# Kernel tuning notes

Measured on AMD Instinct MI355X. Metric: run time of the kernel, lower is better.

## Reference

```python
import jax, jax.numpy as jnp
import numpy as np
import math

B, S, D, H = 2, 2048, 1024, 16


def setup_inputs() -> dict:
    key = jax.random.key(0)
    ks = jax.random.split(key, 5)
    sc = 0.02  # small init scale for weights
    return {
        "x": jax.random.normal(ks[0], (B, S, D), dtype=jnp.float32),
        "Wqkv_w": jax.random.normal(ks[1], (3 * D, D), dtype=jnp.float32) * sc,
        "Wqkv_b": jnp.zeros((3 * D,), jnp.float32),
        "sel_w": jax.random.normal(ks[2], (1, D), dtype=jnp.float32) * sc,
        "sel_b": jnp.zeros((1,), jnp.float32),
        "out_w": jax.random.normal(ks[3], (D, D), dtype=jnp.float32) * sc,
        "out_b": jnp.zeros((D,), jnp.float32),
    }


def reference(x, Wqkv_w, Wqkv_b, sel_w, sel_b, out_w, out_b):
    b, s, d = x.shape
    h = H
    hd = d // h
    # Wqkv projection -> (b, s, 3, h, hd)
    qkv = (x @ Wqkv_w.T + Wqkv_b).reshape(b, s, 3, h, hd)
    q, k, v = qkv[:, :, 0], qkv[:, :, 1], qkv[:, :, 2]
    scale = 1.0 / math.sqrt(hd)
    scores = jnp.einsum('bthd,bshd->bhts', q, k * scale)  # (b,h,s,s)
    causal_mask = jnp.triu(jnp.full((s, s), -10000.0, dtype=scores.dtype), 1)
    attn = jax.nn.softmax(scores + causal_mask, axis=-1)
    ctx = jnp.einsum('bhts,bshd->bthd', attn, v).reshape(b, s, d)
    attn_out = ctx @ out_w.T + out_b  # (b,s,d)
    # selection: softmax over sequence dim, scaled by sqrt(d)/8
    sel = jax.nn.softmax(x @ sel_w.T + sel_b, axis=1) * (math.sqrt(d) / 8.0)  # (b,s,1)
    # eval path: topk over sequence, gather, scatter_add into x
    kk = math.ceil(math.sqrt(s))  # 46 for s=2048
    _, idx = jax.lax.top_k(sel[..., 0], kk)  # (b,kk) indices into seq dim
    val = attn_out * sel  # (b,s,d)
    bidx = jnp.arange(b)[:, None]
    src = val[bidx, idx]  # gather -> (b,kk,d)
    y = x.at[bidx, idx].add(src)  # scatter_add
    return y
```

## Files before the change

### kernel.cpp

```cpp
#include <hip/hip_runtime.h>
#include <stdint.h>

#define BATCH 2
#define SEQ   2048
#define DIM   1024
#define NH    16
#define HD    64
#define KK    46
#define NSEL  (BATCH*KK)
#define MPAD  128
#define CHUNK 128
#define NCH   (SEQ/CHUNK)
#define QP    48
#define SPLITK 8

typedef __attribute__((ext_vector_type(8))) short short8;
typedef __attribute__((ext_vector_type(4))) float f32x4;

__device__ inline unsigned short f2bf(float f) {
  union { float f; uint32_t u; } v; v.f = f;
  uint32_t u = v.u;
  uint32_t r = u + 0x7fff + ((u >> 16) & 1);
  return (unsigned short)(r >> 16);
}
__device__ inline float bf2f(unsigned short h) {
  union { uint32_t u; float f; } v; v.u = ((uint32_t)h) << 16;
  return v.f;
}
__device__ inline uint32_t f2ord(float f) {
  union { float f; uint32_t u; } v; v.f = f;
  return (v.u & 0x80000000u) ? ~v.u : (v.u | 0x80000000u);
}

__device__ inline void gload16(const void* g, void* l) {
  __builtin_amdgcn_global_load_lds(
      (const __attribute__((address_space(1))) void*)g,
      (__attribute__((address_space(3))) void*)l, 16, 0, 0);
}

__global__ void cvtw_kernel(const float* __restrict__ wqkv, const float* __restrict__ outw,
                            unsigned short* __restrict__ wqkvb, unsigned short* __restrict__ outwb) {
  int i = (blockIdx.x * 256 + threadIdx.x) * 8;
  const int NW = 3 * DIM * DIM;
  const float* src; unsigned short* dst; int j;
  if (i < NW) { src = wqkv; dst = wqkvb; j = i; }
  else        { src = outw; dst = outwb; j = i - NW; }
  float4 a = *(const float4*)(src + j);
  float4 b = *(const float4*)(src + j + 4);
  ushort4 o0, o1;
  o0.x = f2bf(a.x); o0.y = f2bf(a.y); o0.z = f2bf(a.z); o0.w = f2bf(a.w);
  o1.x = f2bf(b.x); o1.y = f2bf(b.y); o1.z = f2bf(b.z); o1.w = f2bf(b.w);
  *(ushort4*)(dst + j)     = o0;
  *(ushort4*)(dst + j + 4) = o1;
}

__global__ __launch_bounds__(256) void cvtx_selz_kernel(const float* __restrict__ x,
                                                        unsigned short* __restrict__ xb,
                                                        const float* __restrict__ sel_w,
                                                        const float* __restrict__ sel_b,
                                                        float* __restrict__ z)
{
  int wave = threadIdx.x >> 6, lane = threadIdx.x & 63;
  int row = blockIdx.x * 4 + wave;
  const float* xr = x + (size_t)row * DIM;
  unsigned short* xo = xb + (size_t)row * DIM;
  float s = 0.f;
#pragma unroll
  for (int it = 0; it < 4; ++it) {
    int c = it * 256 + lane * 4;
    float4 xv = *(const float4*)(xr + c);
    float4 wv = *(const float4*)(sel_w + c);
    s += xv.x*wv.x + xv.y*wv.y + xv.z*wv.z + xv.w*wv.w;
    ushort4 o;
    o.x = f2bf(xv.x); o.y = f2bf(xv.y); o.z = f2bf(xv.z); o.w = f2bf(xv.w);
    *(ushort4*)(xo + c) = o;
  }
#pragma unroll
  for (int o = 32; o > 0; o >>= 1) s += __shfl_xor(s, o);
  if (lane == 0) z[row] = s + sel_b[0];
}

__global__ __launch_bounds__(256) void gemm_bt_kernel(
    const unsigned short* __restrict__ A,
    const unsigned short* __restrict__ Bw,
    const float* __restrict__ bias,
    unsigned short* __restrict__ Cout, int M, int N, int K)
{
  __shared__ unsigned short As[2][128*32];
  __shared__ unsigned short Bs[2][128*32];
  int tid  = threadIdx.x;
  int lane = tid & 63, wave = tid >> 6;
  int wr = (wave >> 1) * 64, wc = (wave & 1) * 64;

  int nwg  = gridDim.x * gridDim.y;
  int flat = blockIdx.y * gridDim.x + blockIdx.x;
  int xcd = flat & 7, i8 = flat >> 3;
  int q = nwg >> 3, r = nwg & 7;
  int tile = (xcd < r) ? (xcd * (q + 1) + i8) : (r * (q + 1) + (xcd - r) * q + i8);
  int bx = tile % gridDim.x, by = tile / gridDim.x;
  int bm = by * 128, bn = bx * 128;

  int lr = lane & 15, lk = (lane >> 4) * 8;
  int srow = lane >> 2;
  int scol = (lane & 3) * 8;

  const unsigned short* ap[2];
  const unsigned short* bp[2];
#pragma unroll
  for (int c = 0; c < 2; ++c) {
    int row = (wave * 2 + c) * 16 + srow;
    ap[c] = A  + (size_t)(bm + row) * K + scol;
    bp[c] = Bw + (size_t)(bn + row) * K + scol;
  }

  f32x4 acc[4][4] = {};
  int nt = K / 32;
#pragma unroll
  for (int c = 0; c < 2; ++c) {
    int ch = wave * 2 + c;
    gload16(ap[c], (char*)As[0] + ch * 1024 + lane * 16);
    gload16(bp[c], (char*)Bs[0] + ch * 1024 + lane * 16);
  }
  __syncthreads();

  int cur = 0;
  for (int t = 0; t < nt; ++t) {
    if (t + 1 < nt) {
      int k0 = (t + 1) * 32;
#pragma unroll
      for (int c = 0; c < 2; ++c) {
        int ch = wave * 2 + c;
        gload16(ap[c] + k0, (char*)As[cur ^ 1] + ch * 1024 + lane * 16);
        gload16(bp[c] + k0, (char*)Bs[cur ^ 1] + ch * 1024 + lane * 16);
      }
    }
    short8 af[4], bf[4];
#pragma unroll
    for (int m = 0; m < 4; ++m) af[m] = *(const short8*)&As[cur][(wr + m*16 + lr)*32 + lk];
#pragma unroll
    for (int n = 0; n < 4; ++n) bf[n] = *(const short8*)&Bs[cur][(wc + n*16 + lr)*32 + lk];
#pragma unroll
    for (int m = 0; m < 4; ++m)
#pragma unroll
      for (int n = 0; n < 4; ++n)
        acc[m][n] = __builtin_amdgcn_mfma_f32_16x16x32_bf16(af[m], bf[n], acc[m][n], 0, 0, 0);
    __syncthreads();
    cur ^= 1;
  }

  int rb = 4 * (lane >> 4);
#pragma unroll
  for (int m = 0; m < 4; ++m) {
#pragma unroll
    for (int n = 0; n < 4; ++n) {
      int col = bn + wc + n*16 + lr;
      float bv = bias[col];
#pragma unroll
      for (int i = 0; i < 4; ++i) {
        int row = bm + wr + m*16 + rb + i;
        Cout[(size_t)row * N + col] = f2bf(acc[m][n][i] + bv);
      }
    }
  }
}

template<int GATHER>
__global__ __launch_bounds__(256) void gemm_splitk_kernel(
    const unsigned short* __restrict__ A,
    const unsigned short* __restrict__ Bw,
    float* __restrict__ part, int N, int K,
    const int* __restrict__ idxp)
{
  __shared__ unsigned short As[2][128*32];
  __shared__ unsigned short Bs[2][128*32];
  int tid  = threadIdx.x;
  int lane = tid & 63, wave = tid >> 6;
  int wr = (wave >> 1) * 64, wc = (wave & 1) * 64;
  int bn = blockIdx.x * 128;
  int sk = blockIdx.z;
  int ksl = K / SPLITK;
  int kb  = sk * ksl;

  int lr = lane & 15, lk = (lane >> 4) * 8;
  int srow = lane >> 2;
  int scol = (lane & 3) * 8;

  const unsigned short* ap[2];
  const unsigned short* bp[2];
#pragma unroll
  for (int c = 0; c < 2; ++c) {
    int row = (wave * 2 + c) * 16 + srow;
    size_t arow;
    if (GATHER) {
      int bb = 0, rr = 0;
      if (row < NSEL) { bb = row / KK; rr = idxp[row]; }
      arow = (size_t)(bb * SEQ + rr);
    } else {
      arow = (size_t)row;
    }
    ap[c] = A  + arow * K + kb + scol;
    bp[c] = Bw + (size_t)(bn + row) * K + kb + scol;
  }

  f32x4 acc[4][4] = {};
  int nt = ksl / 32;
#pragma unroll
  for (int c = 0; c < 2; ++c) {
    int ch = wave * 2 + c;
    gload16(ap[c], (char*)As[0] + ch * 1024 + lane * 16);
    gload16(bp[c], (char*)Bs[0] + ch * 1024 + lane * 16);
  }
  __syncthreads();

  int cur = 0;
  for (int t = 0; t < nt; ++t) {
    if (t + 1 < nt) {
      int k0 = (t + 1) * 32;
#pragma unroll
      for (int c = 0; c < 2; ++c) {
        int ch = wave * 2 + c;
        gload16(ap[c] + k0, (char*)As[cur ^ 1] + ch * 1024 + lane * 16);
        gload16(bp[c] + k0, (char*)Bs[cur ^ 1] + ch * 1024 + lane * 16);
      }
    }
    short8 af[4], bf[4];
#pragma unroll
    for (int m = 0; m < 4; ++m) af[m] = *(const short8*)&As[cur][(wr + m*16 + lr)*32 + lk];
#pragma unroll
    for (int n = 0; n < 4; ++n) bf[n] = *(const short8*)&Bs[cur][(wc + n*16 + lr)*32 + lk];
#pragma unroll
    for (int m = 0; m < 4; ++m)
#pragma unroll
      for (int n = 0; n < 4; ++n)
        acc[m][n] = __builtin_amdgcn_mfma_f32_16x16x32_bf16(af[m], bf[n], acc[m][n], 0, 0, 0);
    __syncthreads();
    cur ^= 1;
  }

  int rb = 4 * (lane >> 4);
  float* po = part + (size_t)sk * MPAD * N;
#pragma unroll
  for (int m = 0; m < 4; ++m) {
#pragma unroll
    for (int n = 0; n < 4; ++n) {
      int col = bn + wc + n*16 + lr;
#pragma unroll
      for (int i = 0; i < 4; ++i) {
        int row = wr + m*16 + rb + i;
        po[(size_t)row * N + col] = acc[m][n][i];
      }
    }
  }
}

__global__ void qcombine_kernel(const float* __restrict__ part,
                                const float* __restrict__ bias,
                                unsigned short* __restrict__ qgb)
{
  int i = (blockIdx.x * 256 + threadIdx.x) * 4;
  int col = i & (DIM - 1);
  float4 a = *(const float4*)(bias + col);
#pragma unroll
  for (int sk = 0; sk < SPLITK; ++sk) {
    float4 p = *(const float4*)(part + (size_t)sk * MPAD * DIM + i);
    a.x += p.x; a.y += p.y; a.z += p.z; a.w += p.w;
  }
  ushort4 o;
  o.x = f2bf(a.x); o.y = f2bf(a.y); o.z = f2bf(a.z); o.w = f2bf(a.w);
  *(ushort4*)(qgb + i) = o;
}

__global__ __launch_bounds__(256) void topk_kernel(const float* __restrict__ z,
                                                   float* __restrict__ sel,
                                                   int* __restrict__ idxout,
                                                   int* __restrict__ rowmap)
{
  int b = blockIdx.x, t = threadIdx.x;
  int lane = t & 63, wid = t >> 6;
  __shared__ int   hist[256];
  __shared__ float fred[4];
  __shared__ int   ired[4];
  __shared__ int   s_B, s_need;
  __shared__ float s_mx, s_sum;

  int s0 = t * 8;
  float zz[8];
  uint32_t uu[8];
  {
    float4 a = *(const float4*)(z + b*SEQ + s0);
    float4 c = *(const float4*)(z + b*SEQ + s0 + 4);
    zz[0]=a.x; zz[1]=a.y; zz[2]=a.z; zz[3]=a.w;
    zz[4]=c.x; zz[5]=c.y; zz[6]=c.z; zz[7]=c.w;
  }
#pragma unroll
  for (int i = 0; i < 8; ++i) uu[i] = f2ord(zz[i]);

  float lm = zz[0];
#pragma unroll
  for (int i = 1; i < 8; ++i) lm = fmaxf(lm, zz[i]);
#pragma unroll
  for (int o = 32; o > 0; o >>= 1) lm = fmaxf(lm, __shfl_xor(lm, o));
  if (lane == 0) fred[wid] = lm;
  __syncthreads();
  if (t == 0) s_mx = fmaxf(fmaxf(fred[0], fred[1]), fmaxf(fred[2], fred[3]));
  __syncthreads();
  float mx = s_mx;

  float pp[8];
  float ls = 0.f;
#pragma unroll
  for (int i = 0; i < 8; ++i) { pp[i] = __expf(zz[i] - mx); ls += pp[i]; }
#pragma unroll
  for (int o = 32; o > 0; o >>= 1) ls += __shfl_xor(ls, o);
  if (lane == 0) fred[wid] = ls;
  __syncthreads();
  if (t == 0) s_sum = fred[0] + fred[1] + fred[2] + fred[3];
  __syncthreads();
  float sscale = 4.0f / s_sum;
#pragma unroll
  for (int i = 0; i < 8; ++i) sel[b*SEQ + s0 + i] = pp[i] * sscale;

  uint32_t pref = 0;
  int need = KK;
#pragma unroll
  for (int pass = 0; pass < 4; ++pass) {
    int shift = 24 - pass * 8;
    uint32_t maskhi = pass ? (0xFFFFFFFFu << (shift + 8)) : 0u;
    hist[t] = 0;
    __syncthreads();
#pragma unroll
    for (int i = 0; i < 8; ++i) {
      if ((uu[i] & maskhi) == pref)
        atomicAdd(&hist[(uu[i] >> shift) & 255], 1);
    }
    __syncthreads();
    if (t < 64) {
      int c0 = hist[t*4], c1 = hist[t*4+1], c2 = hist[t*4+2], c3 = hist[t*4+3];
      int sl = c0 + c1 + c2 + c3;
      int suf = sl;
#pragma unroll
      for (int off = 1; off < 64; off <<= 1) {
        int o = __shfl_down(suf, off);
        if (lane + off < 64) suf += o;
      }
      int above = suf - sl;
      if (above < need && above + sl >= need) {
        int cum = above;
        int cs[4] = {c0, c1, c2, c3};
#pragma unroll
        for (int k = 3; k >= 0; --k) {
          if (cum < need && cum + cs[k] >= need) {
            s_B = t*4 + k;
            s_need = need - cum;
            break;
          }
          cum += cs[k];
        }
      }
    }
    __syncthreads();
    pref |= ((uint32_t)s_B) << shift;
    need = s_need;
    __syncthreads();
  }
  uint32_t T = pref;

  int cgt = 0, ceq = 0;
#pragma unroll
  for (int i = 0; i < 8; ++i) { cgt += (uu[i] > T); ceq += (uu[i] == T); }
  int pack = (cgt << 12) | ceq;
  int inc = pack;
#pragma unroll
  for (int off = 1; off < 64; off <<= 1) {
    int o = __shfl_up(inc, off);
    if (lane >= off) inc += o;
  }
  if (lane == 63) ired[wid] = inc;
  __syncthreads();
  int wbase = 0;
  if (wid == 1) wbase = ired[0];
  else if (wid == 2) wbase = ired[0] + ired[1];
  else if (wid == 3) wbase = ired[0] + ired[1] + ired[2];
  int ex = wbase + inc - pack;
  int g = ex >> 12, e = ex & 0xFFF;
#pragma unroll
  for (int i = 0; i < 8; ++i) {
    int s = s0 + i;
    bool isgt = uu[i] > T;
    bool iseq = uu[i] == T;
    int rank = -1;
    if (isgt) rank = g + (e < need ? e : need);
    else if (iseq && e < need) rank = g + e;
    if (rank >= 0) {
      int j = b*KK + rank;
      idxout[j] = s;
      rowmap[b*SEQ + s] = j;
    } else {
      rowmap[b*SEQ + s] = -1;
    }
    g += isgt; e += iseq;
  }
}

__global__ __launch_bounds__(256) void attn_chunk_kernel(
    const unsigned short* __restrict__ qgb,
    const unsigned short* __restrict__ kvb,
    const int* __restrict__ idx,
    float* __restrict__ Opart,
    float* __restrict__ mpart,
    float* __restrict__ lpart)
{
  int h = blockIdx.x, b = blockIdx.y, kc = blockIdx.z;
  int t = threadIdx.x, lane = t & 63, w = t >> 6;
  int lr = lane & 15, hk = lane >> 4;

  __shared__ unsigned short Qs[QP][72];
  __shared__ union { unsigned short Ks[CHUNK][72]; unsigned short ps[QP][136]; } U;
  __shared__ unsigned short Vt[HD][134];
  __shared__ int   rsi[QP];
  __shared__ float wred[4][QP];
  __shared__ float wsum[4][QP];

  if (t < QP) rsi[t] = (t < KK) ? idx[b*KK + t] : -1;
  for (int i = t; i < QP*8; i += 256) {
    int q = i >> 3, c8 = (i & 7) * 8;
    uint4 v;
    if (q < KK) v = *(const uint4*)(qgb + (size_t)(b*KK + q)*DIM + h*HD + c8);
    else        { v.x = 0; v.y = 0; v.z = 0; v.w = 0; }
    *(uint4*)&Qs[q][c8] = v;
  }
  for (int i = t; i < CHUNK*8; i += 256) {
    int r = i >> 3, c8 = (i & 7) * 8;
    *(uint4*)&U.Ks[r][c8] =
      *(const uint4*)(kvb + ((size_t)(b*SEQ + kc*CHUNK + r))*2048 + h*HD + c8);
  }
  for (int i = t; i < CHUNK*8; i += 256) {
    int r = i >> 3, d8 = (i & 7) * 8;
    uint4 v = *(const uint4*)(kvb + ((size_t)(b*SEQ + kc*CHUNK + r))*2048 + DIM + h*HD + d8);
    const unsigned short* pv = (const unsigned short*)&v;
#pragma unroll
    for (int j = 0; j < 8; ++j) Vt[d8 + j][r] = pv[j];
  }
  __syncthreads();

  short8 af[3][2], bfr[2][2];
#pragma unroll
  for (int m = 0; m < 3; ++m)
#pragma unroll
    for (int kk = 0; kk < 2; ++kk)
      af[m][kk] = *(const short8*)&Qs[m*16 + lr][kk*32 + hk*8];
#pragma unroll
  for (int j = 0; j < 2; ++j)
#pragma unroll
    for (int kk = 0; kk < 2; ++kk)
      bfr[j][kk] = *(const short8*)&U.Ks[(2*w + j)*16 + lr][kk*32 + hk*8];
  f32x4 acc[3][2] = {};
#pragma unroll
  for (int kk = 0; kk < 2; ++kk)
#pragma unroll
    for (int m = 0; m < 3; ++m)
#pragma unroll
      for (int j = 0; j < 2; ++j)
        acc[m][j] = __builtin_amdgcn_mfma_f32_16x16x32_bf16(af[m][kk], bfr[j][kk], acc[m][j], 0, 0, 0);

  float s[3][2][4];
  float rmax[3][4];
#pragma unroll
  for (int m = 0; m < 3; ++m)
#pragma unroll
    for (int reg = 0; reg < 4; ++reg) {
      int row = m*16 + hk*4 + reg;
      int rq = rsi[row];
      float mx = -3e38f;
#pragma unroll
      for (int j = 0; j < 2; ++j) {
        int gkey = kc*CHUNK + (2*w + j)*16 + lr;
        float v = acc[m][j][reg] * 0.125f;
        if (gkey > rq) v = -3e38f;
        s[m][j][reg] = v;
        mx = fmaxf(mx, v);
      }
#pragma unroll
      for (int o = 1; o < 16; o <<= 1) mx = fmaxf(mx, __shfl_xor(mx, o));
      rmax[m][reg] = mx;
    }
  if (lr == 0) {
#pragma unroll
    for (int m = 0; m < 3; ++m)
#pragma unroll
      for (int reg = 0; reg < 4; ++reg)
        wred[w][m*16 + hk*4 + reg] = rmax[m][reg];
  }
  __syncthreads();

  float rsum[3][4];
#pragma unroll
  for (int m = 0; m < 3; ++m)
#pragma unroll
    for (int reg = 0; reg < 4; ++reg) {
      int row = m*16 + hk*4 + reg;
      float gm = fmaxf(fmaxf(wred[0][row], wred[1][row]), fmaxf(wred[2][row], wred[3][row]));
      gm = fmaxf(gm, -1e37f);
      float sum = 0.f;
#pragma unroll
      for (int j = 0; j < 2; ++j) {
        float p = __expf(s[m][j][reg] - gm);
        sum += p;
        U.ps[row][(2*w + j)*16 + lr] = f2bf(p);
      }
#pragma unroll
      for (int o = 1; o < 16; o <<= 1) sum += __shfl_xor(sum, o);
      rsum[m][reg] = sum;
      rmax[m][reg] = gm;
    }
  if (lr == 0) {
#pragma unroll
    for (int m = 0; m < 3; ++m)
#pragma unroll
      for (int reg = 0; reg < 4; ++reg)
        wsum[w][m*16 + hk*4 + reg] = rsum[m][reg];
  }
  __syncthreads();

  if (w == 0 && lr == 0) {
    size_t base = ((size_t)(b*NH + h)*NCH + kc)*KK;
#pragma unroll
    for (int m = 0; m < 3; ++m)
#pragma unroll
      for (int reg = 0; reg < 4; ++reg) {
        int row = m*16 + hk*4 + reg;
        if (row < KK) {
          float L = wsum[0][row] + wsum[1][row] + wsum[2][row] + wsum[3][row];
          mpart[base + row] = rmax[m][reg];
          lpart[base + row] = L;
        }
      }
  }

  f32x4 acc2[3] = {};
#pragma unroll
  for (int kt = 0; kt < 4; ++kt) {
    short8 bv = *(const short8*)&Vt[w*16 + lr][kt*32 + hk*8];
#pragma unroll
    for (int m = 0; m < 3; ++m) {
      short8 av = *(const short8*)&U.ps[m*16 + lr][kt*32 + hk*8];
      acc2[m] = __builtin_amdgcn_mfma_f32_16x16x32_bf16(av, bv, acc2[m], 0, 0, 0);
    }
  }
  size_t obase = (((size_t)(b*NH + h)*NCH + kc)*KK)*HD;
#pragma unroll
  for (int m = 0; m < 3; ++m)
#pragma unroll
    for (int reg = 0; reg < 4; ++reg) {
      int q = m*16 + hk*4 + reg;
      if (q < KK) Opart[obase + (size_t)q*HD + w*16 + lr] = acc2[m][reg];
    }
}

__global__ __launch_bounds__(64) void attn_combine_kernel(
    const float* __restrict__ Opart,
    const float* __restrict__ mpart,
    const float* __restrict__ lpart,
    unsigned short* __restrict__ ctxg)
{
  int h = blockIdx.x, j = blockIdx.y;
  int b = j / KK, q = j % KK;
  int d = threadIdx.x;
  size_t mb = (size_t)(b*NH + h)*NCH;
  float M = -3e38f;
#pragma unroll
  for (int c = 0; c < NCH; ++c) M = fmaxf(M, mpart[(mb + c)*KK + q]);
  float L = 0.f, o = 0.f;
#pragma unroll
  for (int c = 0; c < NCH; ++c) {
    float f = __expf(mpart[(mb + c)*KK + q] - M);
    L += lpart[(mb + c)*KK + q] * f;
    o = fmaf(Opart[((mb + c)*KK + q)*HD + d], f, o);
  }
  ctxg[(size_t)j*DIM + h*HD + d] = f2bf(o / L);
}

__global__ void fused_out_kernel(const float* __restrict__ x,
                                 const float* __restrict__ apart,
                                 const float* __restrict__ out_b,
                                 const float* __restrict__ sel,
                                 const int* __restrict__ rowmap,
                                 float* __restrict__ out)
{
  size_t i = ((size_t)blockIdx.x * 256 + threadIdx.x) * 4;
  int row = (int)(i >> 10);
  int col = (int)(i & 1023);
  float4 v = *(const float4*)(x + i);
  int j = rowmap[row];
  if (j >= 0) {
    float s = sel[row];
    float4 a = *(const float4*)(out_b + col);
#pragma unroll
    for (int sk = 0; sk < SPLITK; ++sk) {
      float4 p = *(const float4*)(apart + ((size_t)sk * MPAD + j) * DIM + col);
      a.x += p.x; a.y += p.y; a.z += p.z; a.w += p.w;
    }
    v.x += a.x * s; v.y += a.y * s; v.z += a.z * s; v.w += a.w * s;
  }
  *(float4*)(out + i) = v;
}

extern "C" void kernel_launch(void* const* d_in, const int* in_sizes, int n_in,
                              void* d_out, int out_size, void* d_ws, size_t ws_size,
                              hipStream_t stream)
{
  (void)in_sizes; (void)n_in; (void)out_size; (void)ws_size;
  const float* x      = (const float*)d_in[0];
  const float* Wqkv_w = (const float*)d_in[1];
  const float* Wqkv_b = (const float*)d_in[2];
  const float* sel_w  = (const float*)d_in[3];
  const float* sel_b  = (const float*)d_in[4];
  const float* out_w  = (const float*)d_in[5];
  const float* out_b  = (const float*)d_in[6];
  float* out = (float*)d_out;
  char* ws = (char*)d_ws;

  unsigned short* xb    = (unsigned short*)(ws);
  unsigned short* wqkvb = (unsigned short*)(ws + (8u  << 20));
  unsigned short* outwb = (unsigned short*)(ws + (14u << 20));
  unsigned short* kvb   = (unsigned short*)(ws + (16u << 20));
  float* z      = (float*)(ws + (32u << 20));
  float* sel    = (float*)(ws + (32u << 20) + (16u << 10));
  int*   idx    = (int*)  (ws + (32u << 20) + (32u << 10));
  int*   rowmap = (int*)  (ws + (32u << 20) + (36u << 10));
  unsigned short* ctxg = (unsigned short*)(ws + (33u << 20) + (256u << 10));
  unsigned short* qgb  = (unsigned short*)(ws + (33u << 20) + (512u << 10));
  float* Opart = (float*)(ws + (35u << 20));
  float* mpart = (float*)(ws + (42u << 20));
  float* lpart = (float*)(ws + (42u << 20) + (256u << 10));
  float* qpart = (float*)(ws + (44u << 20));
  float* apart = (float*)(ws + (48u << 20));

  cvtw_kernel<<<2048, 256, 0, stream>>>(Wqkv_w, out_w, wqkvb, outwb);
  cvtx_selz_kernel<<<BATCH*SEQ/4, 256, 0, stream>>>(x, xb, sel_w, sel_b, z);
  topk_kernel<<<BATCH, 256, 0, stream>>>(z, sel, idx, rowmap);

  dim3 gkv(2048/128, (BATCH*SEQ)/128);
  gemm_bt_kernel<<<gkv, 256, 0, stream>>>(xb, wqkvb + (size_t)DIM*DIM, Wqkv_b + DIM,
                                          kvb, BATCH*SEQ, 2*DIM, DIM);

  dim3 gsk(DIM/128, 1, SPLITK);
  gemm_splitk_kernel<1><<<gsk, 256, 0, stream>>>(xb, wqkvb, qpart, DIM, DIM, idx);
  qcombine_kernel<<<MPAD*DIM/1024, 256, 0, stream>>>(qpart, Wqkv_b, qgb);

  dim3 gac(NH, BATCH, NCH);
  attn_chunk_kernel<<<gac, 256, 0, stream>>>(qgb, kvb, idx, Opart, mpart, lpart);
  dim3 gcb(NH, NSEL);
  attn_combine_kernel<<<gcb, 64, 0, stream>>>(Opart, mpart, lpart, ctxg);

  gemm_splitk_kernel<0><<<gsk, 256, 0, stream>>>(ctxg, outwb, apart, DIM, DIM, nullptr);

  fused_out_kernel<<<BATCH*SEQ*DIM/1024, 256, 0, stream>>>(x, apart, out_b, sel, rowmap, out);
}
```

Baseline: 85.70 us.

## Merge prep kernels, fuse KV and Q GEMMs, copy x early and fix only selected rows

Merges the weight conversion and the x conversion/selection-logit kernels into one launch, and that launch also writes x straight into the output. The KV projection GEMM and the gathered split-K Q GEMM now run in a single launch, removing separate launches and letting the small Q work overlap the large GEMM. The final full-tensor pass that re-read x and a rowmap is replaced by a small kernel that updates only the 92 selected rows, so the rowmap writes are gone. The cost is that the prep kernel now writes the whole output as well, and the fused GEMM grid puts two kinds of blocks with very different lengths in one launch.

```diff
diff --git a/kernel.cpp b/kernel.cpp
--- a/kernel.cpp
+++ b/kernel.cpp
@@ -38,138 +38,324 @@
       (__attribute__((address_space(3))) void*)l, 16, 0, 0);
 }
 
-__global__ void cvtw_kernel(const float* __restrict__ wqkv, const float* __restrict__ outw,
-                            unsigned short* __restrict__ wqkvb, unsigned short* __restrict__ outwb) {
-  int i = (blockIdx.x * 256 + threadIdx.x) * 8;
-  const int NW = 3 * DIM * DIM;
-  const float* src; unsigned short* dst; int j;
-  if (i < NW) { src = wqkv; dst = wqkvb; j = i; }
-  else        { src = outw; dst = outwb; j = i - NW; }
-  float4 a = *(const float4*)(src + j);
-  float4 b = *(const float4*)(src + j + 4);
-  ushort4 o0, o1;
-  o0.x = f2bf(a.x); o0.y = f2bf(a.y); o0.z = f2bf(a.z); o0.w = f2bf(a.w);
-  o1.x = f2bf(b.x); o1.y = f2bf(b.y); o1.z = f2bf(b.z); o1.w = f2bf(b.w);
-  *(ushort4*)(dst + j)     = o0;
-  *(ushort4*)(dst + j + 4) = o1;
-}
-
-__global__ __launch_bounds__(256) void cvtx_selz_kernel(const float* __restrict__ x,
-                                                        unsigned short* __restrict__ xb,
-                                                        const float* __restrict__ sel_w,
-                                                        const float* __restrict__ sel_b,
-                                                        float* __restrict__ z)
-{
-  int wave = threadIdx.x >> 6, lane = threadIdx.x & 63;
-  int row = blockIdx.x * 4 + wave;
-  const float* xr = x + (size_t)row * DIM;
-  unsigned short* xo = xb + (size_t)row * DIM;
-  float s = 0.f;
-#pragma unroll
-  for (int it = 0; it < 4; ++it) {
-    int c = it * 256 + lane * 4;
-    float4 xv = *(const float4*)(xr + c);
-    float4 wv = *(const float4*)(sel_w + c);
-    s += xv.x*wv.x + xv.y*wv.y + xv.z*wv.z + xv.w*wv.w;
-    ushort4 o;
-    o.x = f2bf(xv.x); o.y = f2bf(xv.y); o.z = f2bf(xv.z); o.w = f2bf(xv.w);
-    *(ushort4*)(xo + c) = o;
-  }
-#pragma unroll
-  for (int o = 32; o > 0; o >>= 1) s += __shfl_xor(s, o);
-  if (lane == 0) z[row] = s + sel_b[0];
-}
-
-__global__ __launch_bounds__(256) void gemm_bt_kernel(
-    const unsigned short* __restrict__ A,
-    const unsigned short* __restrict__ Bw,
-    const float* __restrict__ bias,
-    unsigned short* __restrict__ Cout, int M, int N, int K)
+__global__ __launch_bounds__(256) void prep_kernel(
+    const float* __restrict__ wqkv, const float* __restrict__ outw,
+    unsigned short* __restrict__ wqkvb, unsigned short* __restrict__ outwb,
+    const float* __restrict__ x, unsigned short* __restrict__ xb,
+    const float* __restrict__ sel_w, const float* __restrict__ sel_b,
+    float* __restrict__ z, float* __restrict__ out)
+{
+  if (blockIdx.x < 2048) {
+    int i = (blockIdx.x * 256 + threadIdx.x) * 8;
+    const int NW = 3 * DIM * DIM;
+    const float* src; unsigned short* dst; int j;
+    if (i < NW) { src = wqkv; dst = wqkvb; j = i; }
+    else        { src = outw; dst = outwb; j = i - NW; }
+    float4 a = *(const float4*)(src + j);
+    float4 b = *(const float4*)(src + j + 4);
+    ushort4 o0, o1;
+    o0.x = f2bf(a.x); o0.y = f2bf(a.y); o0.z = f2bf(a.z); o0.w = f2bf(a.w);
+    o1.x = f2bf(b.x); o1.y = f2bf(b.y); o1.z = f2bf(b.z); o1.w = f2bf(b.w);
+    *(ushort4*)(dst + j)     = o0;
+    *(ushort4*)(dst + j + 4) = o1;
+  } else {
+    int wave = threadIdx.x >> 6, lane = threadIdx.x & 63;
+    int row = (blockIdx.x - 2048) * 4 + wave;
+    const float* xr = x + (size_t)row * DIM;
+    unsigned short* xo = xb + (size_t)row * DIM;
+    float* oo = out + (size_t)row * DIM;
+    float s = 0.f;
+#pragma unroll
+    for (int it = 0; it < 4; ++it) {
+      int c = it * 256 + lane * 4;
+      float4 xv = *(const float4*)(xr + c);
+      float4 wv = *(const float4*)(sel_w + c);
+      s += xv.x*wv.x + xv.y*wv.y + xv.z*wv.z + xv.w*wv.w;
+      ushort4 o;
+      o.x = f2bf(xv.x); o.y = f2bf(xv.y); o.z = f2bf(xv.z); o.w = f2bf(xv.w);
+      *(ushort4*)(xo + c) = o;
+      *(float4*)(oo + c) = xv;
+    }
+#pragma unroll
+    for (int o = 32; o > 0; o >>= 1) s += __shfl_xor(s, o);
+    if (lane == 0) z[row] = s + sel_b[0];
+  }
+}
+
+__global__ __launch_bounds__(256) void topk_kernel(const float* __restrict__ z,
+                                                   float* __restrict__ sel,
+                                                   int* __restrict__ idxout)
+{
+  int b = blockIdx.x, t = threadIdx.x;
+  int lane = t & 63, wid = t >> 6;
+  __shared__ int   hist[256];
+  __shared__ float fred[4];
+  __shared__ int   ired[4];
+  __shared__ int   s_B, s_need;
+  __shared__ float s_mx, s_sum;
+
+  int s0 = t * 8;
+  float zz[8];
+  uint32_t uu[8];
+  {
+    float4 a = *(const float4*)(z + b*SEQ + s0);
+    float4 c = *(const float4*)(z + b*SEQ + s0 + 4);
+    zz[0]=a.x; zz[1]=a.y; zz[2]=a.z; zz[3]=a.w;
+    zz[4]=c.x; zz[5]=c.y; zz[6]=c.z; zz[7]=c.w;
+  }
+#pragma unroll
+  for (int i = 0; i < 8; ++i) uu[i] = f2ord(zz[i]);
+
+  float lm = zz[0];
+#pragma unroll
+  for (int i = 1; i < 8; ++i) lm = fmaxf(lm, zz[i]);
+#pragma unroll
+  for (int o = 32; o > 0; o >>= 1) lm = fmaxf(lm, __shfl_xor(lm, o));
+  if (lane == 0) fred[wid] = lm;
+  __syncthreads();
+  if (t == 0) s_mx = fmaxf(fmaxf(fred[0], fred[1]), fmaxf(fred[2], fred[3]));
+  __syncthreads();
+  float mx = s_mx;
+
+  float pp[8];
+  float ls = 0.f;
+#pragma unroll
+  for (int i = 0; i < 8; ++i) { pp[i] = __expf(zz[i] - mx); ls += pp[i]; }
+#pragma unroll
+  for (int o = 32; o > 0; o >>= 1) ls += __shfl_xor(ls, o);
+  if (lane == 0) fred[wid] = ls;
+  __syncthreads();
+  if (t == 0) s_sum = fred[0] + fred[1] + fred[2] + fred[3];
+  __syncthreads();
+  float sscale = 4.0f / s_sum;
+#pragma unroll
+  for (int i = 0; i < 8; ++i) sel[b*SEQ + s0 + i] = pp[i] * sscale;
+
+  uint32_t pref = 0;
+  int need = KK;
+#pragma unroll
+  for (int pass = 0; pass < 4; ++pass) {
+    int shift = 24 - pass * 8;
+    uint32_t maskhi = pass ? (0xFFFFFFFFu << (shift + 8)) : 0u;
+    hist[t] = 0;
+    __syncthreads();
+#pragma unroll
+    for (int i = 0; i < 8; ++i) {
+      if ((uu[i] & maskhi) == pref)
+        atomicAdd(&hist[(uu[i] >> shift) & 255], 1);
+    }
+    __syncthreads();
+    if (t < 64) {
+      int c0 = hist[t*4], c1 = hist[t*4+1], c2 = hist[t*4+2], c3 = hist[t*4+3];
+      int sl = c0 + c1 + c2 + c3;
+      int suf = sl;
+#pragma unroll
+      for (int off = 1; off < 64; off <<= 1) {
+        int o = __shfl_down(suf, off);
+        if (lane + off < 64) suf += o;
+      }
+      int above = suf - sl;
+      if (above < need && above + sl >= need) {
+        int cum = above;
+        int cs[4] = {c0, c1, c2, c3};
+#pragma unroll
+        for (int k = 3; k >= 0; --k) {
+          if (cum < need && cum + cs[k] >= need) {
+            s_B = t*4 + k;
+            s_need = need - cum;
+            break;
+          }
+          cum += cs[k];
+        }
+      }
+    }
+    __syncthreads();
+    pref |= ((uint32_t)s_B) << shift;
+    need = s_need;
+    __syncthreads();
+  }
+  uint32_t T = pref;
+
+  int cgt = 0, ceq = 0;
+#pragma unroll
+  for (int i = 0; i < 8; ++i) { cgt += (uu[i] > T); ceq += (uu[i] == T); }
+  int pack = (cgt << 12) | ceq;
+  int inc = pack;
+#pragma unroll
+  for (int off = 1; off < 64; off <<= 1) {
+    int o = __shfl_up(inc, off);
+    if (lane >= off) inc += o;
+  }
+  if (lane == 63) ired[wid] = inc;
+  __syncthreads();
+  int wbase = 0;
+  if (wid == 1) wbase = ired[0];
+  else if (wid == 2) wbase = ired[0] + ired[1];
+  else if (wid == 3) wbase = ired[0] + ired[1] + ired[2];
+  int ex = wbase + inc - pack;
+  int g = ex >> 12, e = ex & 0xFFF;
+#pragma unroll
+  for (int i = 0; i < 8; ++i) {
+    int s = s0 + i;
+    bool isgt = uu[i] > T;
+    bool iseq = uu[i] == T;
+    int rank = -1;
+    if (isgt) rank = g + (e < need ? e : need);
+    else if (iseq && e < need) rank = g + e;
+    if (rank >= 0) idxout[b*KK + rank] = s;
+    g += isgt; e += iseq;
+  }
+}
+
+__global__ __launch_bounds__(256) void gemms_kernel(
+    const unsigned short* __restrict__ xb,
+    const unsigned short* __restrict__ wqkvb,
+    const float* __restrict__ Wqkv_b,
+    unsigned short* __restrict__ kvb,
+    float* __restrict__ qpart,
+    const int* __restrict__ idxp)
 {
   __shared__ unsigned short As[2][128*32];
   __shared__ unsigned short Bs[2][128*32];
   int tid  = threadIdx.x;
   int lane = tid & 63, wave = tid >> 6;
   int wr = (wave >> 1) * 64, wc = (wave & 1) * 64;
-
-  int nwg  = gridDim.x * gridDim.y;
-  int flat = blockIdx.y * gridDim.x + blockIdx.x;
-  int xcd = flat & 7, i8 = flat >> 3;
-  int q = nwg >> 3, r = nwg & 7;
-  int tile = (xcd < r) ? (xcd * (q + 1) + i8) : (r * (q + 1) + (xcd - r) * q + i8);
-  int bx = tile % gridDim.x, by = tile / gridDim.x;
-  int bm = by * 128, bn = bx * 128;
-
   int lr = lane & 15, lk = (lane >> 4) * 8;
   int srow = lane >> 2;
   int scol = (lane & 3) * 8;
-
-  const unsigned short* ap[2];
-  const unsigned short* bp[2];
-#pragma unroll
-  for (int c = 0; c < 2; ++c) {
-    int row = (wave * 2 + c) * 16 + srow;
-    ap[c] = A  + (size_t)(bm + row) * K + scol;
-    bp[c] = Bw + (size_t)(bn + row) * K + scol;
-  }
-
-  f32x4 acc[4][4] = {};
-  int nt = K / 32;
-#pragma unroll
-  for (int c = 0; c < 2; ++c) {
-    int ch = wave * 2 + c;
-    gload16(ap[c], (char*)As[0] + ch * 1024 + lane * 16);
-    gload16(bp[c], (char*)Bs[0] + ch * 1024 + lane * 16);
-  }
-  __syncthreads();
-
-  int cur = 0;
-  for (int t = 0; t < nt; ++t) {
-    if (t + 1 < nt) {
-      int k0 = (t + 1) * 32;
-#pragma unroll
-      for (int c = 0; c < 2; ++c) {
-        int ch = wave * 2 + c;
-        gload16(ap[c] + k0, (char*)As[cur ^ 1] + ch * 1024 + lane * 16);
-        gload16(bp[c] + k0, (char*)Bs[cur ^ 1] + ch * 1024 + lane * 16);
-      }
-    }
-    short8 af[4], bf[4];
-#pragma unroll
-    for (int m = 0; m < 4; ++m) af[m] = *(const short8*)&As[cur][(wr + m*16 + lr)*32 + lk];
-#pragma unroll
-    for (int n = 0; n < 4; ++n) bf[n] = *(const short8*)&Bs[cur][(wc + n*16 + lr)*32 + lk];
-#pragma unroll
-    for (int m = 0; m < 4; ++m)
-#pragma unroll
-      for (int n = 0; n < 4; ++n)
-        acc[m][n] = __builtin_amdgcn_mfma_f32_16x16x32_bf16(af[m], bf[n], acc[m][n], 0, 0, 0);
+  int rb = 4 * (lane >> 4);
+
+  if (blockIdx.x < 512) {
+    const unsigned short* Bw = wqkvb + (size_t)DIM * DIM;
+    int flat = blockIdx.x;
+    int xcd = flat & 7, i8 = flat >> 3;
+    int tile = xcd * 64 + i8;
+    int bx = tile & 15, by = tile >> 4;
+    int bm = by * 128, bn = bx * 128;
+    const int K = DIM, N = 2 * DIM;
+
+    const unsigned short* ap[2];
+    const unsigned short* bp[2];
+#pragma unroll
+    for (int c = 0; c < 2; ++c) {
+      int row = (wave * 2 + c) * 16 + srow;
+      ap[c] = xb + (size_t)(bm + row) * K + scol;
+      bp[c] = Bw + (size_t)(bn + row) * K + scol;
+    }
+    f32x4 acc[4][4] = {};
+#pragma unroll
+    for (int c = 0; c < 2; ++c) {
+      int ch = wave * 2 + c;
+      gload16(ap[c], (char*)As[0] + ch * 1024 + lane * 16);
+      gload16(bp[c], (char*)Bs[0] + ch * 1024 + lane * 16);
+    }
     __syncthreads();
-    cur ^= 1;
-  }
-
-  int rb = 4 * (lane >> 4);
-#pragma unroll
-  for (int m = 0; m < 4; ++m) {
-#pragma unroll
-    for (int n = 0; n < 4; ++n) {
-      int col = bn + wc + n*16 + lr;
-      float bv = bias[col];
-#pragma unroll
-      for (int i = 0; i < 4; ++i) {
-        int row = bm + wr + m*16 + rb + i;
-        Cout[(size_t)row * N + col] = f2bf(acc[m][n][i] + bv);
-      }
-    }
-  }
-}
-
-template<int GATHER>
+    int cur = 0;
+    for (int t = 0; t < 32; ++t) {
+      if (t + 1 < 32) {
+        int k0 = (t + 1) * 32;
+#pragma unroll
+        for (int c = 0; c < 2; ++c) {
+          int ch = wave * 2 + c;
+          gload16(ap[c] + k0, (char*)As[cur ^ 1] + ch * 1024 + lane * 16);
+          gload16(bp[c] + k0, (char*)Bs[cur ^ 1] + ch * 1024 + lane * 16);
+        }
+      }
+      short8 af[4], bf[4];
+#pragma unroll
+      for (int m = 0; m < 4; ++m) af[m] = *(const short8*)&As[cur][(wr + m*16 + lr)*32 + lk];
+#pragma unroll
+      for (int n = 0; n < 4; ++n) bf[n] = *(const short8*)&Bs[cur][(wc + n*16 + lr)*32 + lk];
+#pragma unroll
+      for (int m = 0; m < 4; ++m)
+#pragma unroll
+        for (int n = 0; n < 4; ++n)
+          acc[m][n] = __builtin_amdgcn_mfma_f32_16x16x32_bf16(af[m], bf[n], acc[m][n], 0, 0, 0);
+      __syncthreads();
+      cur ^= 1;
+    }
+#pragma unroll
+    for (int m = 0; m < 4; ++m) {
+#pragma unroll
+      for (int n = 0; n < 4; ++n) {
+        int col = bn + wc + n*16 + lr;
+        float bv = Wqkv_b[DIM + col];
+#pragma unroll
+        for (int i = 0; i < 4; ++i) {
+          int row = bm + wr + m*16 + rb + i;
+          kvb[(size_t)row * N + col] = f2bf(acc[m][n][i] + bv);
+        }
+      }
+    }
+  } else {
+    int bi = blockIdx.x - 512;
+    int sk = bi >> 3;
+    int bn = (bi & 7) * 128;
+    int kb = sk * 128;
+    const int K = DIM, N = DIM;
+
+    const unsigned short* ap[2];
+    const unsigned short* bp[2];
+#pragma unroll
+    for (int c = 0; c < 2; ++c) {
+      int row = (wave * 2 + c) * 16 + srow;
+      int bb = 0, rr = 0;
+      if (row < NSEL) { bb = row / KK; rr = idxp[row]; }
+      ap[c] = xb + ((size_t)(bb * SEQ + rr)) * K + kb + scol;
+      bp[c] = wqkvb + (size_t)(bn + row) * K + kb + scol;
+    }
+    f32x4 acc[4][4] = {};
+#pragma unroll
+    for (int c = 0; c < 2; ++c) {
+      int ch = wave * 2 + c;
+      gload16(ap[c], (char*)As[0] + ch * 1024 + lane * 16);
+      gload16(bp[c], (char*)Bs[0] + ch * 1024 + lane * 16);
+    }
+    __syncthreads();
+    int cur = 0;
+    for (int t = 0; t < 4; ++t) {
+      if (t + 1 < 4) {
+        int k0 = (t + 1) * 32;
+#pragma unroll
+        for (int c = 0; c < 2; ++c) {
+          int ch = wave * 2 + c;
+          gload16(ap[c] + k0, (char*)As[cur ^ 1] + ch * 1024 + lane * 16);
+          gload16(bp[c] + k0, (char*)Bs[cur ^ 1] + ch * 1024 + lane * 16);
+        }
+      }
+      short8 af[4], bf[4];
+#pragma unroll
+      for (int m = 0; m < 4; ++m) af[m] = *(const short8*)&As[cur][(wr + m*16 + lr)*32 + lk];
+#pragma unroll
+      for (int n = 0; n < 4; ++n) bf[n] = *(const short8*)&Bs[cur][(wc + n*16 + lr)*32 + lk];
+#pragma unroll
+      for (int m = 0; m < 4; ++m)
+#pragma unroll
+        for (int n = 0; n < 4; ++n)
+          acc[m][n] = __builtin_amdgcn_mfma_f32_16x16x32_bf16(af[m], bf[n], acc[m][n], 0, 0, 0);
+      __syncthreads();
+      cur ^= 1;
+    }
+    float* po = qpart + (size_t)sk * MPAD * N;
+#pragma unroll
+    for (int m = 0; m < 4; ++m) {
+#pragma unroll
+      for (int n = 0; n < 4; ++n) {
+        int col = bn + wc + n*16 + lr;
+#pragma unroll
+        for (int i = 0; i < 4; ++i) {
+          int row = wr + m*16 + rb + i;
+          po[(size_t)row * N + col] = acc[m][n][i];
+        }
+      }
+    }
+  }
+}
+
 __global__ __launch_bounds__(256) void gemm_splitk_kernel(
     const unsigned short* __restrict__ A,
     const unsigned short* __restrict__ Bw,
-    float* __restrict__ part, int N, int K,
-    const int* __restrict__ idxp)
+    float* __restrict__ part, int N, int K)
 {
   __shared__ unsigned short As[2][128*32];
   __shared__ unsigned short Bs[2][128*32];
@@ -190,15 +376,7 @@
 #pragma unroll
   for (int c = 0; c < 2; ++c) {
     int row = (wave * 2 + c) * 16 + srow;
-    size_t arow;
-    if (GATHER) {
-      int bb = 0, rr = 0;
-      if (row < NSEL) { bb = row / KK; rr = idxp[row]; }
-      arow = (size_t)(bb * SEQ + rr);
-    } else {
-      arow = (size_t)row;
-    }
-    ap[c] = A  + arow * K + kb + scol;
+    ap[c] = A  + (size_t)row * K + kb + scol;
     bp[c] = Bw + (size_t)(bn + row) * K + kb + scol;
   }
 
@@ -268,138 +446,6 @@
   ushort4 o;
   o.x = f2bf(a.x); o.y = f2bf(a.y); o.z = f2bf(a.z); o.w = f2bf(a.w);
   *(ushort4*)(qgb + i) = o;
-}
-
-__global__ __launch_bounds__(256) void topk_kernel(const float* __restrict__ z,
-                                                   float* __restrict__ sel,
-                                                   int* __restrict__ idxout,
-                                                   int* __restrict__ rowmap)
-{
-  int b = blockIdx.x, t = threadIdx.x;
-  int lane = t & 63, wid = t >> 6;
-  __shared__ int   hist[256];
-  __shared__ float fred[4];
-  __shared__ int   ired[4];
-  __shared__ int   s_B, s_need;
-  __shared__ float s_mx, s_sum;
-
-  int s0 = t * 8;
-  float zz[8];
-  uint32_t uu[8];
-  {
-    float4 a = *(const float4*)(z + b*SEQ + s0);
-    float4 c = *(const float4*)(z + b*SEQ + s0 + 4);
-    zz[0]=a.x; zz[1]=a.y; zz[2]=a.z; zz[3]=a.w;
-    zz[4]=c.x; zz[5]=c.y; zz[6]=c.z; zz[7]=c.w;
-  }
-#pragma unroll
-  for (int i = 0; i < 8; ++i) uu[i] = f2ord(zz[i]);
-
-  float lm = zz[0];
-#pragma unroll
-  for (int i = 1; i < 8; ++i) lm = fmaxf(lm, zz[i]);
-#pragma unroll
-  for (int o = 32; o > 0; o >>= 1) lm = fmaxf(lm, __shfl_xor(lm, o));
-  if (lane == 0) fred[wid] = lm;
-  __syncthreads();
-  if (t == 0) s_mx = fmaxf(fmaxf(fred[0], fred[1]), fmaxf(fred[2], fred[3]));
-  __syncthreads();
-  float mx = s_mx;
-
-  float pp[8];
-  float ls = 0.f;
-#pragma unroll
-  for (int i = 0; i < 8; ++i) { pp[i] = __expf(zz[i] - mx); ls += pp[i]; }
-#pragma unroll
-  for (int o = 32; o > 0; o >>= 1) ls += __shfl_xor(ls, o);
-  if (lane == 0) fred[wid] = ls;
-  __syncthreads();
-  if (t == 0) s_sum = fred[0] + fred[1] + fred[2] + fred[3];
-  __syncthreads();
-  float sscale = 4.0f / s_sum;
-#pragma unroll
-  for (int i = 0; i < 8; ++i) sel[b*SEQ + s0 + i] = pp[i] * sscale;
-
-  uint32_t pref = 0;
-  int need = KK;
-#pragma unroll
-  for (int pass = 0; pass < 4; ++pass) {
-    int shift = 24 - pass * 8;
-    uint32_t maskhi = pass ? (0xFFFFFFFFu << (shift + 8)) : 0u;
-    hist[t] = 0;
-    __syncthreads();
-#pragma unroll
-    for (int i = 0; i < 8; ++i) {
-      if ((uu[i] & maskhi) == pref)
-        atomicAdd(&hist[(uu[i] >> shift) & 255], 1);
-    }
-    __syncthreads();
-    if (t < 64) {
-      int c0 = hist[t*4], c1 = hist[t*4+1], c2 = hist[t*4+2], c3 = hist[t*4+3];
-      int sl = c0 + c1 + c2 + c3;
-      int suf = sl;
-#pragma unroll
-      for (int off = 1; off < 64; off <<= 1) {
-        int o = __shfl_down(suf, off);
-        if (lane + off < 64) suf += o;
-      }
-      int above = suf - sl;
-      if (above < need && above + sl >= need) {
-        int cum = above;
-        int cs[4] = {c0, c1, c2, c3};
-#pragma unroll
-        for (int k = 3; k >= 0; --k) {
-          if (cum < need && cum + cs[k] >= need) {
-            s_B = t*4 + k;
-            s_need = need - cum;
-            break;
-          }
-          cum += cs[k];
-        }
-      }
-    }
-    __syncthreads();
-    pref |= ((uint32_t)s_B) << shift;
-    need = s_need;
-    __syncthreads();
-  }
-  uint32_t T = pref;
-
-  int cgt = 0, ceq = 0;
-#pragma unroll
-  for (int i = 0; i < 8; ++i) { cgt += (uu[i] > T); ceq += (uu[i] == T); }
-  int pack = (cgt << 12) | ceq;
-  int inc = pack;
-#pragma unroll
-  for (int off = 1; off < 64; off <<= 1) {
-    int o = __shfl_up(inc, off);
-    if (lane >= off) inc += o;
-  }
-  if (lane == 63) ired[wid] = inc;
-  __syncthreads();
-  int wbase = 0;
-  if (wid == 1) wbase = ired[0];
-  else if (wid == 2) wbase = ired[0] + ired[1];
-  else if (wid == 3) wbase = ired[0] + ired[1] + ired[2];
-  int ex = wbase + inc - pack;
-  int g = ex >> 12, e = ex & 0xFFF;
-#pragma unroll
-  for (int i = 0; i < 8; ++i) {
-    int s = s0 + i;
-    bool isgt = uu[i] > T;
-    bool iseq = uu[i] == T;
-    int rank = -1;
-    if (isgt) rank = g + (e < need ? e : need);
-    else if (iseq && e < need) rank = g + e;
-    if (rank >= 0) {
-      int j = b*KK + rank;
-      idxout[j] = s;
-      rowmap[b*SEQ + s] = j;
-    } else {
-      rowmap[b*SEQ + s] = -1;
-    }
-    g += isgt; e += iseq;
-  }
 }
 
 __global__ __launch_bounds__(256) void attn_chunk_kernel(
@@ -580,29 +626,28 @@
   ctxg[(size_t)j*DIM + h*HD + d] = f2bf(o / L);
 }
 
-__global__ void fused_out_kernel(const float* __restrict__ x,
-                                 const float* __restrict__ apart,
-                                 const float* __restrict__ out_b,
-                                 const float* __restrict__ sel,
-                                 const int* __restrict__ rowmap,
-                                 float* __restrict__ out)
-{
-  size_t i = ((size_t)blockIdx.x * 256 + threadIdx.x) * 4;
-  int row = (int)(i >> 10);
-  int col = (int)(i & 1023);
-  float4 v = *(const float4*)(x + i);
-  int j = rowmap[row];
-  if (j >= 0) {
-    float s = sel[row];
-    float4 a = *(const float4*)(out_b + col);
-#pragma unroll
-    for (int sk = 0; sk < SPLITK; ++sk) {
-      float4 p = *(const float4*)(apart + ((size_t)sk * MPAD + j) * DIM + col);
-      a.x += p.x; a.y += p.y; a.z += p.z; a.w += p.w;
-    }
-    v.x += a.x * s; v.y += a.y * s; v.z += a.z * s; v.w += a.w * s;
-  }
-  *(float4*)(out + i) = v;
+__global__ void rowfix_kernel(const float* __restrict__ x,
+                              const float* __restrict__ apart,
+                              const float* __restrict__ out_b,
+                              const float* __restrict__ sel,
+                              const int* __restrict__ idx,
+                              float* __restrict__ out)
+{
+  int j = blockIdx.x;
+  int b = j / KK;
+  int r = idx[j];
+  int col = threadIdx.x * 4;
+  size_t off = ((size_t)(b * SEQ + r)) * DIM + col;
+  float s = sel[b * SEQ + r];
+  float4 a = *(const float4*)(out_b + col);
+#pragma unroll
+  for (int sk = 0; sk < SPLITK; ++sk) {
+    float4 p = *(const float4*)(apart + ((size_t)sk * MPAD + j) * DIM + col);
+    a.x += p.x; a.y += p.y; a.z += p.z; a.w += p.w;
+  }
+  float4 v = *(const float4*)(x + off);
+  v.x += a.x * s; v.y += a.y * s; v.z += a.z * s; v.w += a.w * s;
+  *(float4*)(out + off) = v;
 }
 
 extern "C" void kernel_launch(void* const* d_in, const int* in_sizes, int n_in,
@@ -627,7 +672,6 @@
   float* z      = (float*)(ws + (32u << 20));
   float* sel    = (float*)(ws + (32u << 20) + (16u << 10));
   int*   idx    = (int*)  (ws + (32u << 20) + (32u << 10));
-  int*   rowmap = (int*)  (ws + (32u << 20) + (36u << 10));
   unsigned short* ctxg = (unsigned short*)(ws + (33u << 20) + (256u << 10));
   unsigned short* qgb  = (unsigned short*)(ws + (33u << 20) + (512u << 10));
   float* Opart = (float*)(ws + (35u << 20));
@@ -636,16 +680,11 @@
   float* qpart = (float*)(ws + (44u << 20));
   float* apart = (float*)(ws + (48u << 20));
 
-  cvtw_kernel<<<2048, 256, 0, stream>>>(Wqkv_w, out_w, wqkvb, outwb);
-  cvtx_selz_kernel<<<BATCH*SEQ/4, 256, 0, stream>>>(x, xb, sel_w, sel_b, z);
-  topk_kernel<<<BATCH, 256, 0, stream>>>(z, sel, idx, rowmap);
-
-  dim3 gkv(2048/128, (BATCH*SEQ)/128);
-  gemm_bt_kernel<<<gkv, 256, 0, stream>>>(xb, wqkvb + (size_t)DIM*DIM, Wqkv_b + DIM,
-                                          kvb, BATCH*SEQ, 2*DIM, DIM);
-
-  dim3 gsk(DIM/128, 1, SPLITK);
-  gemm_splitk_kernel<1><<<gsk, 256, 0, stream>>>(xb, wqkvb, qpart, DIM, DIM, idx);
+  prep_kernel<<<3072, 256, 0, stream>>>(Wqkv_w, out_w, wqkvb, outwb,
+                                        x, xb, sel_w, sel_b, z, out);
+  topk_kernel<<<BATCH, 256, 0, stream>>>(z, sel, idx);
+
+  gemms_kernel<<<576, 256, 0, stream>>>(xb, wqkvb, Wqkv_b, kvb, qpart, idx);
   qcombine_kernel<<<MPAD*DIM/1024, 256, 0, stream>>>(qpart, Wqkv_b, qgb);
 
   dim3 gac(NH, BATCH, NCH);
@@ -653,7 +692,8 @@
   dim3 gcb(NH, NSEL);
   attn_combine_kernel<<<gcb, 64, 0, stream>>>(Opart, mpart, lpart, ctxg);
 
-  gemm_splitk_kernel<0><<<gsk, 256, 0, stream>>>(ctxg, outwb, apart, DIM, DIM, nullptr);
-
-  fused_out_kernel<<<BATCH*SEQ*DIM/1024, 256, 0, stream>>>(x, apart, out_b, sel, rowmap, out);
-}
+  dim3 gsk(DIM/128, 1, SPLITK);
+  gemm_splitk_kernel<<<gsk, 256, 0, stream>>>(ctxg, outwb, apart, DIM, DIM);
+
+  rowfix_kernel<<<NSEL, 256, 0, stream>>>(x, apart, out_b, sel, idx, out);
+}
```

Result: faster. 77.02 us (-10.1%).
